# Kernel optimization log

Measured on AMD Instinct MI355X. Metric: run time of the kernel, lower is better.

Reference implementation:

```python
import jax, jax.numpy as jnp
import numpy as np

B, C, H, W = 8, 512, 32, 32
EMB, HEADS, GROUPS = 512, 8, 32
DH = EMB // HEADS
EPS = 1e-5


def setup_inputs() -> dict:
    key = jax.random.key(0)
    ks = jax.random.split(key, 11)
    s_in = 1.0 / np.sqrt(C)
    s_emb = 1.0 / np.sqrt(EMB)
    return {
        "x": jax.random.normal(ks[0], (B, C, H, W), jnp.float32),
        "Wq": jax.random.uniform(ks[1], (C, EMB), jnp.float32, -s_in, s_in),
        "bq": jax.random.uniform(ks[2], (EMB,), jnp.float32, -s_in, s_in),
        "Wk": jax.random.uniform(ks[3], (C, EMB), jnp.float32, -s_in, s_in),
        "bk": jax.random.uniform(ks[4], (EMB,), jnp.float32, -s_in, s_in),
        "Wv": jax.random.uniform(ks[5], (C, EMB), jnp.float32, -s_in, s_in),
        "bv": jax.random.uniform(ks[6], (EMB,), jnp.float32, -s_in, s_in),
        "Wo": jax.random.uniform(ks[7], (EMB, EMB), jnp.float32, -s_emb, s_emb),
        "bo": jax.random.uniform(ks[8], (EMB,), jnp.float32, -s_emb, s_emb),
        "gn_w": jnp.ones((EMB,), jnp.float32),
        "gn_b": jnp.zeros((EMB,), jnp.float32),
    }


def _group_norm(y, w, b):
    # y: [B, C, H, W]; normalize within each of GROUPS channel groups over (C//G, H, W)
    b_, c_, h_, w_ = y.shape
    yg = y.reshape(b_, GROUPS, c_ // GROUPS, h_, w_)
    mean = yg.mean(axis=(2, 3, 4), keepdims=True)
    var = yg.var(axis=(2, 3, 4), keepdims=True)
    yg = (yg - mean) * jax.lax.rsqrt(var + EPS)
    y = yg.reshape(b_, c_, h_, w_)
    return y * w[None, :, None, None] + b[None, :, None, None]


def reference(x, Wq, bq, Wk, bk, Wv, bv, Wo, bo, gn_w, gn_b):
    b, c, h, w = x.shape
    s = h * w
    xs = x.reshape(b, c, s).transpose(0, 2, 1)  # [B, S, C]
    # QKV projections, split into heads: [B, heads, S, dh]
    def heads(t):
        return t.reshape(b, s, HEADS, DH).transpose(0, 2, 1, 3)
    q = heads(xs @ Wq + bq)
    k = heads(xs @ Wk + bk)
    v = heads(xs @ Wv + bv)
    scale = DH ** -0.5
    scores = jnp.einsum('bhqd,bhkd->bhqk', q, k) * scale  # [B, heads, S, S]
    attn = jax.nn.softmax(scores, axis=-1)
    out = jnp.einsum('bhqk,bhkd->bhqd', attn, v)  # [B, heads, S, dh]
    out = out.transpose(0, 2, 1, 3).reshape(b, s, EMB)  # concat heads
    proj = out @ Wo + bo  # [B, S, EMB]
    proj = proj.transpose(0, 2, 1).reshape(b, EMB, h, w)
    return _group_norm(proj + x, gn_w, gn_b)
```

## Files before the change

### kernel.cpp

```cpp
#include <hip/hip_runtime.h>

#define BB 8
#define CC 512
#define SS 1024
#define EMB 512
#define HEADS 8
#define DH 64
#define GROUPS 32
#define CPG 16
#define EPS 1e-5f

typedef __bf16 bf16x8 __attribute__((ext_vector_type(8)));
typedef __bf16 bf16x4 __attribute__((ext_vector_type(4)));
typedef float f32x4 __attribute__((ext_vector_type(4)));
typedef unsigned short u16x4 __attribute__((ext_vector_type(4)));

__device__ inline unsigned short f2bf(float f) {
    union { float f; unsigned u; } c; c.f = f;
    unsigned u = c.u + 0x7FFF + ((c.u >> 16) & 1);
    return (unsigned short)(u >> 16);
}

#if defined(__has_builtin)
#if __has_builtin(__builtin_amdgcn_exp2f)
#define EXP2F(x) __builtin_amdgcn_exp2f(x)
#endif
#endif
#ifndef EXP2F
#define EXP2F(x) __expf(0.69314718f * (x))
#endif

#define MFMA16(a, b, c) __builtin_amdgcn_mfma_f32_16x16x32_bf16((a), (b), (c), 0, 0, 0)
#define GLOAD_LDS16(g, s)                                                     \
    __builtin_amdgcn_global_load_lds(                                         \
        (const __attribute__((address_space(1))) void*)(g),                   \
        (__attribute__((address_space(3))) void*)(s), 16, 0, 0)

__global__ __launch_bounds__(256) void prep_x(
    const float* __restrict__ x, unsigned short* __restrict__ xT)
{
    __shared__ float tile[32][33];
    const int s0 = blockIdx.x * 32;
    const int c0 = blockIdx.y * 32;
    const int b  = blockIdx.z;
    const int t  = threadIdx.x;

    {
        int c = t >> 3, s4 = (t & 7) * 4;
        float4 v = *(const float4*)(x + ((size_t)b * CC + c0 + c) * SS + s0 + s4);
        tile[c][s4] = v.x; tile[c][s4 + 1] = v.y;
        tile[c][s4 + 2] = v.z; tile[c][s4 + 3] = v.w;
    }
    __syncthreads();
    {
        int sr = t >> 3, c4 = (t & 7) * 4;
        u16x4 o;
        #pragma unroll
        for (int i = 0; i < 4; ++i) o[i] = f2bf(tile[c4 + i][sr]);
        *(u16x4*)(xT + ((size_t)(b << 10) + s0 + sr) * CC + c0 + c4) = o;
    }
}

__global__ __launch_bounds__(256) void prep_w(
    const float* __restrict__ Wq, const float* __restrict__ Wk,
    const float* __restrict__ Wv, const float* __restrict__ Wo,
    unsigned short* __restrict__ Wt)
{
    __shared__ float tile[32][33];
    const int z = blockIdx.z;
    const float* W = (z == 0) ? Wq : (z == 1) ? Wk : (z == 2) ? Wv : Wo;
    unsigned short* dst = Wt + (size_t)z * EMB * CC;
    const int k0 = blockIdx.x * 32;
    const int n0 = blockIdx.y * 32;
    const int t  = threadIdx.x;

    {
        int k = t >> 3, n4 = (t & 7) * 4;
        float4 v = *(const float4*)(W + (size_t)(k0 + k) * EMB + n0 + n4);
        tile[k][n4] = v.x; tile[k][n4 + 1] = v.y;
        tile[k][n4 + 2] = v.z; tile[k][n4 + 3] = v.w;
    }
    __syncthreads();
    {
        int n = t >> 3, k4 = (t & 7) * 4;
        u16x4 o;
        #pragma unroll
        for (int i = 0; i < 4; ++i) o[i] = f2bf(tile[k4 + i][n]);
        *(u16x4*)(dst + (size_t)(n0 + n) * CC + k0 + k4) = o;
    }
}

#define GEMM_CORE(Aptr, Bptr)                                                  \
    __shared__ __align__(16) char lds[32768];                                  \
    const int t = threadIdx.x, w = t >> 6, l = t & 63;                         \
    const int wr = w >> 1, wc = w & 1;                                         \
    const int rl = l & 15, kh = l >> 4;                                        \
    f32x4 acc[4][4] = {};                                                      \
    {                                                                          \
        const int srow = w * 32 + (l >> 2);                                    \
        const int sslot = (l & 3) ^ ((srow >> 1) & 3);                         \
        const char* Ag0 = (const char*)(Aptr) + (size_t)(m0 + srow) * 1024 + sslot * 16;      \
        const char* Ag1 = (const char*)(Aptr) + (size_t)(m0 + srow + 16) * 1024 + (((l & 3) ^ (((srow + 16) >> 1) & 3)) * 16); \
        const char* Bg0 = (const char*)(Bptr) + (size_t)(n0 + srow) * 1024 + sslot * 16;      \
        const char* Bg1 = (const char*)(Bptr) + (size_t)(n0 + srow + 16) * 1024 + (((l & 3) ^ (((srow + 16) >> 1) & 3)) * 16); \
        for (int kt = 0; kt < 16; ++kt) {                                      \
            if (kt == 0) {                                                     \
                GLOAD_LDS16(Ag0, lds + w * 2048);                              \
                GLOAD_LDS16(Ag1, lds + w * 2048 + 1024);                       \
                GLOAD_LDS16(Bg0, lds + 8192 + w * 2048);                       \
                GLOAD_LDS16(Bg1, lds + 8192 + w * 2048 + 1024);                \
                __syncthreads();                                               \
            }                                                                  \
            const int buf = kt & 1;                                            \
            if (kt < 15) {                                                     \
                const int kb = (kt + 1) * 64;                                  \
                char* Al = lds + (buf ^ 1) * 16384;                            \
                char* Bl = Al + 8192;                                          \
                GLOAD_LDS16(Ag0 + kb, Al + w * 2048);                          \
                GLOAD_LDS16(Ag1 + kb, Al + w * 2048 + 1024);                   \
                GLOAD_LDS16(Bg0 + kb, Bl + w * 2048);                          \
                GLOAD_LDS16(Bg1 + kb, Bl + w * 2048 + 1024);                   \
            }                                                                  \
            const char* Al = lds + buf * 16384;                                \
            const char* Bl = Al + 8192;                                        \
            bf16x8 af[4], bfr[4];                                              \
            _Pragma("unroll")                                                  \
            for (int i = 0; i < 4; ++i) {                                      \
                int row = wr * 64 + i * 16 + rl;                               \
                af[i] = *(const bf16x8*)(Al + row * 64 + ((kh ^ ((row >> 1) & 3)) << 4)); \
                int col = wc * 64 + i * 16 + rl;                               \
                bfr[i] = *(const bf16x8*)(Bl + col * 64 + ((kh ^ ((col >> 1) & 3)) << 4)); \
            }                                                                  \
            _Pragma("unroll")                                                  \
            for (int i = 0; i < 4; ++i)                                        \
                _Pragma("unroll")                                              \
                for (int j = 0; j < 4; ++j)                                    \
                    acc[i][j] = MFMA16(af[i], bfr[j], acc[i][j]);              \
            __syncthreads();                                                   \
        }                                                                      \
    }

__global__ __launch_bounds__(256) void qkv_mm(
    const unsigned short* __restrict__ xT, const unsigned short* __restrict__ Wt,
    const float* __restrict__ bq, const float* __restrict__ bk,
    const float* __restrict__ bv,
    unsigned short* __restrict__ Qb, unsigned short* __restrict__ Kb,
    unsigned short* __restrict__ Vb)
{
    const int z = blockIdx.z;
    const unsigned short* Bt = Wt + (size_t)z * EMB * CC;
    const float* bias = (z == 0) ? bq : (z == 1) ? bk : bv;
    const int m0 = blockIdx.x * 128, n0 = blockIdx.y * 128;

    GEMM_CORE(xT, Bt)

    if (z == 2) {
        #pragma unroll
        for (int i = 0; i < 4; ++i) {
            #pragma unroll
            for (int j = 0; j < 4; ++j) {
                int n = n0 + wc * 64 + j * 16 + rl;
                int h = n >> 6, d = n & 63;
                float bi = bias[n];
                int mb = m0 + wr * 64 + i * 16 + kh * 4;
                int b = mb >> 10, s = mb & 1023;
                bf16x4 o;
                #pragma unroll
                for (int r = 0; r < 4; ++r) o[r] = (__bf16)(acc[i][j][r] + bi);
                *(bf16x4*)((__bf16*)Vb + (((size_t)(b * HEADS + h)) * DH + d) * SS + s) = o;
            }
        }
    } else {
        unsigned short* outp = (z == 0) ? Qb : Kb;
        #pragma unroll
        for (int i = 0; i < 4; ++i) {
            #pragma unroll
            for (int j = 0; j < 4; ++j) {
                int n = n0 + wc * 64 + j * 16 + rl;
                int h = n >> 6, d = n & 63;
                float bi = bias[n];
                #pragma unroll
                for (int r = 0; r < 4; ++r) {
                    int m = m0 + wr * 64 + i * 16 + kh * 4 + r;
                    int b = m >> 10, s = m & 1023;
                    outp[(((size_t)(b * HEADS + h)) * SS + s) * DH + d] =
                        f2bf(acc[i][j][r] + bi);
                }
            }
        }
    }
}

__global__ __launch_bounds__(256) void proj_mm(
    const unsigned short* __restrict__ AO, const unsigned short* __restrict__ Wot,
    const float* __restrict__ bo, const float* __restrict__ x,
    float* __restrict__ Y)
{
    const int m0 = blockIdx.x * 128, n0 = blockIdx.y * 128;

    GEMM_CORE(AO, Wot)

    #pragma unroll
    for (int i = 0; i < 4; ++i) {
        #pragma unroll
        for (int j = 0; j < 4; ++j) {
            int n = n0 + wc * 64 + j * 16 + rl;
            float bi = bo[n];
            int mb = m0 + wr * 64 + i * 16 + kh * 4;
            int b = mb >> 10, s = mb & 1023;
            const float4 xr = *(const float4*)(x + ((size_t)b * CC + n) * SS + s);
            float4 o;
            o.x = acc[i][j][0] + bi + xr.x;
            o.y = acc[i][j][1] + bi + xr.y;
            o.z = acc[i][j][2] + bi + xr.z;
            o.w = acc[i][j][3] + bi + xr.w;
            *(float4*)(Y + ((size_t)b * CC + n) * SS + s) = o;
        }
    }
}

__global__ __launch_bounds__(256) void attn_mfma(
    const unsigned short* __restrict__ Q, const unsigned short* __restrict__ K,
    const unsigned short* __restrict__ V, unsigned short* __restrict__ Aout)
{
    __shared__ __align__(16) char lds[40960];

    const int wg  = blockIdx.x;
    const int xcd = wg & 7;
    const int idx = wg >> 3;
    const int pair = xcd * 8 + (idx >> 4);
    const int qb   = idx & 15;
    const int h = pair & 7;
    const int b = pair >> 3;
    const int q0 = qb * 64;

    const size_t kbase = ((size_t)b * HEADS + h) * SS * DH;
    const size_t vbase = ((size_t)b * HEADS + h) * DH * SS;

    const int t  = threadIdx.x;
    const int w  = t >> 6;
    const int l  = t & 63;
    const int g  = l >> 4;
    const int qi = l & 15;
    char* Pl = lds + 32768 + w * 2048;

    bf16x8 qf[2];
    {
        const unsigned short* qrow = Q + kbase + (size_t)(q0 + w * 16 + qi) * DH;
        qf[0] = *(const bf16x8*)(qrow + g * 8);
        qf[1] = *(const bf16x8*)(qrow + 32 + g * 8);
    }

    const int srow = t >> 3;
    const int seg  = t & 7;
    const unsigned short* kg0 = K + kbase + (size_t)srow * DH + ((seg ^ (srow & 7)) * 8);
    const unsigned short* vg0 = V + vbase + (size_t)srow * SS + ((seg ^ (srow & 7)) * 8);

#define ATTN_STAGE(bb, ktn)                                                    \
    GLOAD_LDS16(kg0 + (ktn) * 4096, lds + (bb) + t * 16);                      \
    GLOAD_LDS16(kg0 + (ktn) * 4096 + 2048, lds + (bb) + 4096 + t * 16);        \
    GLOAD_LDS16(vg0 + (ktn) * 64, lds + (bb) + 8192 + t * 16);                 \
    GLOAD_LDS16(vg0 + (ktn) * 64 + 32768, lds + (bb) + 12288 + t * 16);

    f32x4 O[4] = {};
    float m2 = -1e30f, lsum = 0.f;
    const float cscale = 0.125f * 1.44269504f;

    int bufb = 0;
    ATTN_STAGE(0, 0)
    __syncthreads();

    for (int kt = 0; kt < 16; ++kt) {
        if (kt < 15) { ATTN_STAGE(bufb ^ 16384, kt + 1) }

        const char* Kl = lds + bufb;
        const char* Vl = lds + bufb + 8192;

        f32x4 st[4] = {};
        __builtin_amdgcn_s_setprio(1);
        #pragma unroll
        for (int tt = 0; tt < 4; ++tt) {
            int row = tt * 16 + qi;
            #pragma unroll
            for (int c = 0; c < 2; ++c) {
                bf16x8 kf = *(const bf16x8*)(Kl + row * 128 +
                              ((c * 64 + g * 16) ^ ((row & 7) << 4)));
                st[tt] = MFMA16(kf, qf[c], st[tt]);
            }
        }
        __builtin_amdgcn_s_setprio(0);

        float tv[16];
        float pmax = -1e30f;
        #pragma unroll
        for (int tt = 0; tt < 4; ++tt)
            #pragma unroll
            for (int r = 0; r < 4; ++r) {
                float v = st[tt][r] * cscale;
                tv[tt * 4 + r] = v;
                pmax = fmaxf(pmax, v);
            }
        if (!__all(pmax <= m2 + 8.0f)) {
            float gm = fmaxf(pmax, __shfl_xor(pmax, 16));
            gm = fmaxf(gm, __shfl_xor(gm, 32));
            float newm = fmaxf(m2, gm);
            float alpha = EXP2F(m2 - newm);
            #pragma unroll
            for (int dt = 0; dt < 4; ++dt)
                #pragma unroll
                for (int r = 0; r < 4; ++r) O[dt][r] *= alpha;
            lsum *= alpha;
            m2 = newm;
        }
        #pragma unroll
        for (int tt = 0; tt < 4; ++tt) {
            bf16x4 pk;
            #pragma unroll
            for (int r = 0; r < 4; ++r) {
                float p = EXP2F(tv[tt * 4 + r] - m2);
                lsum += p;
                pk[r] = (__bf16)p;
            }
            *(bf16x4*)(Pl + qi * 128 + ((tt * 32 + g * 8) ^ ((qi & 7) << 4))) = pk;
        }

        bf16x8 pf0 = *(const bf16x8*)(Pl + qi * 128 + ((g * 16) ^ ((qi & 7) << 4)));
        bf16x8 pf1 = *(const bf16x8*)(Pl + qi * 128 + ((64 + g * 16) ^ ((qi & 7) << 4)));
        __builtin_amdgcn_s_setprio(1);
        #pragma unroll
        for (int dt = 0; dt < 4; ++dt) {
            int d = dt * 16 + qi;
            bf16x8 vf0 = *(const bf16x8*)(Vl + d * 128 + ((g * 16) ^ ((d & 7) << 4)));
            O[dt] = MFMA16(vf0, pf0, O[dt]);
            bf16x8 vf1 = *(const bf16x8*)(Vl + d * 128 + ((64 + g * 16) ^ ((d & 7) << 4)));
            O[dt] = MFMA16(vf1, pf1, O[dt]);
        }
        __builtin_amdgcn_s_setprio(0);

        __syncthreads();
        bufb ^= 16384;
    }

    lsum += __shfl_xor(lsum, 16);
    lsum += __shfl_xor(lsum, 32);
    const float inv = __builtin_amdgcn_rcpf(lsum);
    unsigned short* orow = Aout + ((size_t)b * SS + q0 + w * 16 + qi) * EMB + h * DH;
    #pragma unroll
    for (int dt = 0; dt < 4; ++dt) {
        bf16x4 o;
        #pragma unroll
        for (int r = 0; r < 4; ++r) o[r] = (__bf16)(O[dt][r] * inv);
        *(bf16x4*)((__bf16*)orow + dt * 16 + g * 4) = o;
    }
#undef ATTN_STAGE
}

__global__ __launch_bounds__(256) void gnorm2(
    const float* __restrict__ Y, const float* __restrict__ gw,
    const float* __restrict__ gb, float* __restrict__ out)
{
    __shared__ float red[8];
    __shared__ float stats[2];

    const int grp = blockIdx.x;
    const int b   = blockIdx.y;
    const int t   = threadIdx.x;
    const size_t base = ((size_t)b * CC + grp * CPG) * SS;

    float sum = 0.f, sq = 0.f;
    #pragma unroll
    for (int i = 0; i < 16; ++i) {
        float4 v = *(const float4*)(Y + base + (size_t)(t + i * 256) * 4);
        sum += v.x + v.y + v.z + v.w;
        sq  += v.x * v.x + v.y * v.y + v.z * v.z + v.w * v.w;
    }
    #pragma unroll
    for (int off = 32; off; off >>= 1) {
        sum += __shfl_down(sum, off);
        sq  += __shfl_down(sq, off);
    }
    const int wid = t >> 6;
    if ((t & 63) == 0) { red[wid] = sum; red[4 + wid] = sq; }
    __syncthreads();
    if (t == 0) {
        float s1 = red[0] + red[1] + red[2] + red[3];
        float s2 = red[4] + red[5] + red[6] + red[7];
        float mean = s1 / (float)(CPG * SS);
        float var  = s2 / (float)(CPG * SS) - mean * mean;
        stats[0] = mean;
        stats[1] = rsqrtf(var + EPS);
    }
    __syncthreads();
    const float mean = stats[0], rs = stats[1];

    #pragma unroll
    for (int i = 0; i < 16; ++i) {
        size_t idx = (size_t)(t + i * 256) * 4;
        int ch = grp * CPG + (int)(idx >> 10);
        float wgt = gw[ch], bet = gb[ch];
        float4 v = *(const float4*)(Y + base + idx);
        float4 o;
        o.x = (v.x - mean) * rs * wgt + bet;
        o.y = (v.y - mean) * rs * wgt + bet;
        o.z = (v.z - mean) * rs * wgt + bet;
        o.w = (v.w - mean) * rs * wgt + bet;
        *(float4*)(out + base + idx) = o;
    }
}

extern "C" void kernel_launch(void* const* d_in, const int* in_sizes, int n_in,
                              void* d_out, int out_size, void* d_ws, size_t ws_size,
                              hipStream_t stream) {
    const float* x   = (const float*)d_in[0];
    const float* Wq  = (const float*)d_in[1];
    const float* bq  = (const float*)d_in[2];
    const float* Wk  = (const float*)d_in[3];
    const float* bk  = (const float*)d_in[4];
    const float* Wv  = (const float*)d_in[5];
    const float* bv  = (const float*)d_in[6];
    const float* Wo  = (const float*)d_in[7];
    const float* bo  = (const float*)d_in[8];
    const float* gnw = (const float*)d_in[9];
    const float* gnb = (const float*)d_in[10];
    float* out = (float*)d_out;
    char* ws  = (char*)d_ws;

    unsigned short* xT  = (unsigned short*)(ws);
    unsigned short* Wt  = (unsigned short*)(ws + 8388608);
    unsigned short* Qb  = (unsigned short*)(ws + 10485760);
    unsigned short* Kb  = (unsigned short*)(ws + 18874368);
    unsigned short* Vb  = (unsigned short*)(ws + 27262976);
    unsigned short* AO  = (unsigned short*)(ws + 35651584);
    float*          Y   = (float*)(ws + 44040192);

    prep_x<<<dim3(32, 16, 8), 256, 0, stream>>>(x, xT);
    prep_w<<<dim3(16, 16, 4), 256, 0, stream>>>(Wq, Wk, Wv, Wo, Wt);
    qkv_mm<<<dim3(64, 4, 3), 256, 0, stream>>>(xT, Wt, bq, bk, bv, Qb, Kb, Vb);
    attn_mfma<<<dim3(1024), 256, 0, stream>>>(Qb, Kb, Vb, AO);
    proj_mm<<<dim3(64, 4), 256, 0, stream>>>(AO, Wt + (size_t)3 * EMB * CC, bo, x, Y);
    gnorm2<<<dim3(32, 8), 256, 0, stream>>>(Y, gnw, gnb, out);
}
```

Baseline: 91.10 us.

## Double query rows per attention wave to reuse K/V tiles across two sub-blocks

Each attention workgroup now handles 128 query rows instead of 64: every wave processes two 16-row query sub-tiles that share the K and V fragments loaded from LDS, and the grid is halved. This halves global K/V traffic and LDS reads per query and doubles MFMA work per fragment load, at the cost of more registers and a larger LDS P buffer, which may reduce occupancy. The Q/K store in the QKV GEMM also swaps the manual bf16 rounding helper for a native bf16 conversion.

```diff
diff --git a/kernel.cpp b/kernel.cpp
--- a/kernel.cpp
+++ b/kernel.cpp
@@ -183,8 +183,8 @@
                 for (int r = 0; r < 4; ++r) {
                     int m = m0 + wr * 64 + i * 16 + kh * 4 + r;
                     int b = m >> 10, s = m & 1023;
-                    outp[(((size_t)(b * HEADS + h)) * SS + s) * DH + d] =
-                        f2bf(acc[i][j][r] + bi);
+                    ((__bf16*)outp)[(((size_t)(b * HEADS + h)) * SS + s) * DH + d] =
+                        (__bf16)(acc[i][j][r] + bi);
                 }
             }
         }
@@ -223,16 +223,16 @@
     const unsigned short* __restrict__ Q, const unsigned short* __restrict__ K,
     const unsigned short* __restrict__ V, unsigned short* __restrict__ Aout)
 {
-    __shared__ __align__(16) char lds[40960];
+    __shared__ __align__(16) char lds[49152];
 
     const int wg  = blockIdx.x;
     const int xcd = wg & 7;
     const int idx = wg >> 3;
-    const int pair = xcd * 8 + (idx >> 4);
-    const int qb   = idx & 15;
+    const int pair = xcd * 8 + (idx >> 3);
+    const int qb   = idx & 7;
     const int h = pair & 7;
     const int b = pair >> 3;
-    const int q0 = qb * 64;
+    const int q0 = qb * 128;
 
     const size_t kbase = ((size_t)b * HEADS + h) * SS * DH;
     const size_t vbase = ((size_t)b * HEADS + h) * DH * SS;
@@ -242,13 +242,15 @@
     const int l  = t & 63;
     const int g  = l >> 4;
     const int qi = l & 15;
-    char* Pl = lds + 32768 + w * 2048;
-
-    bf16x8 qf[2];
-    {
-        const unsigned short* qrow = Q + kbase + (size_t)(q0 + w * 16 + qi) * DH;
-        qf[0] = *(const bf16x8*)(qrow + g * 8);
-        qf[1] = *(const bf16x8*)(qrow + 32 + g * 8);
+    char* Pl = lds + 32768 + w * 4096;
+
+    bf16x8 qf[2][2];
+    #pragma unroll
+    for (int u = 0; u < 2; ++u) {
+        const unsigned short* qrow =
+            Q + kbase + (size_t)(q0 + w * 32 + u * 16 + qi) * DH;
+        qf[u][0] = *(const bf16x8*)(qrow + g * 8);
+        qf[u][1] = *(const bf16x8*)(qrow + 32 + g * 8);
     }
 
     const int srow = t >> 3;
@@ -262,8 +264,9 @@
     GLOAD_LDS16(vg0 + (ktn) * 64, lds + (bb) + 8192 + t * 16);                 \
     GLOAD_LDS16(vg0 + (ktn) * 64 + 32768, lds + (bb) + 12288 + t * 16);
 
-    f32x4 O[4] = {};
-    float m2 = -1e30f, lsum = 0.f;
+    f32x4 O[4][2] = {};
+    float m2[2]   = {-1e30f, -1e30f};
+    float lsum[2] = {0.f, 0.f};
     const float cscale = 0.125f * 1.44269504f;
 
     int bufb = 0;
@@ -276,64 +279,80 @@
         const char* Kl = lds + bufb;
         const char* Vl = lds + bufb + 8192;
 
-        f32x4 st[4] = {};
+        f32x4 st[4][2] = {};
         __builtin_amdgcn_s_setprio(1);
         #pragma unroll
         for (int tt = 0; tt < 4; ++tt) {
             int row = tt * 16 + qi;
-            #pragma unroll
-            for (int c = 0; c < 2; ++c) {
-                bf16x8 kf = *(const bf16x8*)(Kl + row * 128 +
-                              ((c * 64 + g * 16) ^ ((row & 7) << 4)));
-                st[tt] = MFMA16(kf, qf[c], st[tt]);
+            bf16x8 kf0 = *(const bf16x8*)(Kl + row * 128 +
+                          ((g * 16) ^ ((row & 7) << 4)));
+            bf16x8 kf1 = *(const bf16x8*)(Kl + row * 128 +
+                          ((64 + g * 16) ^ ((row & 7) << 4)));
+            #pragma unroll
+            for (int u = 0; u < 2; ++u) {
+                st[tt][u] = MFMA16(kf0, qf[u][0], st[tt][u]);
+                st[tt][u] = MFMA16(kf1, qf[u][1], st[tt][u]);
             }
         }
         __builtin_amdgcn_s_setprio(0);
 
-        float tv[16];
-        float pmax = -1e30f;
+        float pmax[2] = {-1e30f, -1e30f};
         #pragma unroll
         for (int tt = 0; tt < 4; ++tt)
             #pragma unroll
-            for (int r = 0; r < 4; ++r) {
-                float v = st[tt][r] * cscale;
-                tv[tt * 4 + r] = v;
-                pmax = fmaxf(pmax, v);
-            }
-        if (!__all(pmax <= m2 + 8.0f)) {
-            float gm = fmaxf(pmax, __shfl_xor(pmax, 16));
-            gm = fmaxf(gm, __shfl_xor(gm, 32));
-            float newm = fmaxf(m2, gm);
-            float alpha = EXP2F(m2 - newm);
-            #pragma unroll
-            for (int dt = 0; dt < 4; ++dt)
+            for (int u = 0; u < 2; ++u)
                 #pragma unroll
-                for (int r = 0; r < 4; ++r) O[dt][r] *= alpha;
-            lsum *= alpha;
-            m2 = newm;
-        }
-        #pragma unroll
-        for (int tt = 0; tt < 4; ++tt) {
-            bf16x4 pk;
-            #pragma unroll
-            for (int r = 0; r < 4; ++r) {
-                float p = EXP2F(tv[tt * 4 + r] - m2);
-                lsum += p;
-                pk[r] = (__bf16)p;
-            }
-            *(bf16x4*)(Pl + qi * 128 + ((tt * 32 + g * 8) ^ ((qi & 7) << 4))) = pk;
-        }
-
-        bf16x8 pf0 = *(const bf16x8*)(Pl + qi * 128 + ((g * 16) ^ ((qi & 7) << 4)));
-        bf16x8 pf1 = *(const bf16x8*)(Pl + qi * 128 + ((64 + g * 16) ^ ((qi & 7) << 4)));
+                for (int r = 0; r < 4; ++r) {
+                    float v = st[tt][u][r] * cscale;
+                    st[tt][u][r] = v;
+                    pmax[u] = fmaxf(pmax[u], v);
+                }
+        #pragma unroll
+        for (int u = 0; u < 2; ++u) {
+            if (!__all(pmax[u] <= m2[u] + 8.0f)) {
+                float gm = fmaxf(pmax[u], __shfl_xor(pmax[u], 16));
+                gm = fmaxf(gm, __shfl_xor(gm, 32));
+                float newm = fmaxf(m2[u], gm);
+                float alpha = EXP2F(m2[u] - newm);
+                #pragma unroll
+                for (int dt = 0; dt < 4; ++dt)
+                    #pragma unroll
+                    for (int r = 0; r < 4; ++r) O[dt][u][r] *= alpha;
+                lsum[u] *= alpha;
+                m2[u] = newm;
+            }
+            #pragma unroll
+            for (int tt = 0; tt < 4; ++tt) {
+                bf16x4 pk;
+                #pragma unroll
+                for (int r = 0; r < 4; ++r) {
+                    float p = EXP2F(st[tt][u][r] - m2[u]);
+                    lsum[u] += p;
+                    pk[r] = (__bf16)p;
+                }
+                *(bf16x4*)(Pl + u * 2048 + qi * 128 +
+                           ((tt * 32 + g * 8) ^ ((qi & 7) << 4))) = pk;
+            }
+        }
+
+        bf16x8 pf[2][2];
+        #pragma unroll
+        for (int u = 0; u < 2; ++u)
+            #pragma unroll
+            for (int hh = 0; hh < 2; ++hh)
+                pf[u][hh] = *(const bf16x8*)(Pl + u * 2048 + qi * 128 +
+                             ((hh * 64 + g * 16) ^ ((qi & 7) << 4)));
         __builtin_amdgcn_s_setprio(1);
         #pragma unroll
         for (int dt = 0; dt < 4; ++dt) {
             int d = dt * 16 + qi;
             bf16x8 vf0 = *(const bf16x8*)(Vl + d * 128 + ((g * 16) ^ ((d & 7) << 4)));
-            O[dt] = MFMA16(vf0, pf0, O[dt]);
             bf16x8 vf1 = *(const bf16x8*)(Vl + d * 128 + ((64 + g * 16) ^ ((d & 7) << 4)));
-            O[dt] = MFMA16(vf1, pf1, O[dt]);
+            #pragma unroll
+            for (int u = 0; u < 2; ++u) {
+                O[dt][u] = MFMA16(vf0, pf[u][0], O[dt][u]);
+                O[dt][u] = MFMA16(vf1, pf[u][1], O[dt][u]);
+            }
         }
         __builtin_amdgcn_s_setprio(0);
 
@@ -341,16 +360,21 @@
         bufb ^= 16384;
     }
 
-    lsum += __shfl_xor(lsum, 16);
-    lsum += __shfl_xor(lsum, 32);
-    const float inv = __builtin_amdgcn_rcpf(lsum);
-    unsigned short* orow = Aout + ((size_t)b * SS + q0 + w * 16 + qi) * EMB + h * DH;
-    #pragma unroll
-    for (int dt = 0; dt < 4; ++dt) {
-        bf16x4 o;
-        #pragma unroll
-        for (int r = 0; r < 4; ++r) o[r] = (__bf16)(O[dt][r] * inv);
-        *(bf16x4*)((__bf16*)orow + dt * 16 + g * 4) = o;
+    #pragma unroll
+    for (int u = 0; u < 2; ++u) {
+        float ls = lsum[u];
+        ls += __shfl_xor(ls, 16);
+        ls += __shfl_xor(ls, 32);
+        const float inv = __builtin_amdgcn_rcpf(ls);
+        unsigned short* orow = Aout +
+            ((size_t)b * SS + q0 + w * 32 + u * 16 + qi) * EMB + h * DH;
+        #pragma unroll
+        for (int dt = 0; dt < 4; ++dt) {
+            bf16x4 o;
+            #pragma unroll
+            for (int r = 0; r < 4; ++r) o[r] = (__bf16)(O[dt][u][r] * inv);
+            *(bf16x4*)((__bf16*)orow + dt * 16 + g * 4) = o;
+        }
     }
 #undef ATTN_STAGE
 }
@@ -436,7 +460,7 @@
     prep_x<<<dim3(32, 16, 8), 256, 0, stream>>>(x, xT);
     prep_w<<<dim3(16, 16, 4), 256, 0, stream>>>(Wq, Wk, Wv, Wo, Wt);
     qkv_mm<<<dim3(64, 4, 3), 256, 0, stream>>>(xT, Wt, bq, bk, bv, Qb, Kb, Vb);
-    attn_mfma<<<dim3(1024), 256, 0, stream>>>(Qb, Kb, Vb, AO);
+    attn_mfma<<<dim3(512), 256, 0, stream>>>(Qb, Kb, Vb, AO);
     proj_mm<<<dim3(64, 4), 256, 0, stream>>>(AO, Wt + (size_t)3 * EMB * CC, bo, x, Y);
     gnorm2<<<dim3(32, 8), 256, 0, stream>>>(Y, gnw, gnb, out);
 }
```

After: 87.10 us. 4.4% less time.
